# Performance work log

Hardware: AMD Instinct MI355X
Metric: run time of the kernel (lower is better)

## Reference

```python
import jax, jax.numpy as jnp
import numpy as np

N = 50000
E = 800000
IN_C = 128
HID = 64
HEADS = 4
EPS = 1e-5
NEG_SLOPE = 0.2


def _glorot(key, shape, fan_in):
    return jax.random.normal(key, shape, dtype=jnp.float32) / np.sqrt(fan_in)


def setup_inputs() -> dict:
    key = jax.random.key(0)
    ks = jax.random.split(key, 32)
    d = {}
    d["x"] = jax.random.normal(ks[0], (N, IN_C), dtype=jnp.float32)
    d["edge_index"] = jax.random.randint(ks[1], (2, E), 0, N, dtype=jnp.int32)
    ph = HID // HEADS  # per-head channels for concat layers (16)
    # Layer 1: in -> [heads, ph], concat
    d["W1"] = _glorot(ks[2], (IN_C, HEADS * ph), IN_C)
    d["a1s"] = _glorot(ks[3], (HEADS, ph), ph)
    d["a1d"] = _glorot(ks[4], (HEADS, ph), ph)
    d["b1"] = jnp.zeros((HID,), jnp.float32)
    # Layer 2: hid -> [heads, ph], concat
    d["W2"] = _glorot(ks[5], (HID, HEADS * ph), HID)
    d["a2s"] = _glorot(ks[6], (HEADS, ph), ph)
    d["a2d"] = _glorot(ks[7], (HEADS, ph), ph)
    d["b2"] = jnp.zeros((HID,), jnp.float32)
    # Layer 3: hid -> [heads, HID], mean over heads (concat=False)
    d["W3"] = _glorot(ks[8], (HID, HEADS * HID), HID)
    d["a3s"] = _glorot(ks[9], (HEADS, HID), HID)
    d["a3d"] = _glorot(ks[10], (HEADS, HID), HID)
    d["b3"] = jnp.zeros((HID,), jnp.float32)
    # BatchNorms (eval mode: running stats)
    for i, k0 in zip((1, 2, 3), (11, 14, 17)):
        d[f"bn{i}_g"] = jnp.ones((HID,), jnp.float32)
        d[f"bn{i}_b"] = jnp.zeros((HID,), jnp.float32)
        d[f"bn{i}_m"] = 0.1 * jax.random.normal(ks[k0], (HID,), dtype=jnp.float32)
        d[f"bn{i}_v"] = jax.random.uniform(ks[k0 + 1], (HID,), minval=0.5, maxval=1.5, dtype=jnp.float32)
    # Classifier MLP: HID -> HID//2 -> 1
    d["cW1"] = _glorot(ks[20], (HID, HID // 2), HID)
    d["cb1"] = jnp.zeros((HID // 2,), jnp.float32)
    d["cW2"] = _glorot(ks[21], (HID // 2, 1), HID // 2)
    d["cb2"] = jnp.zeros((1,), jnp.float32)
    return d


def _gat_layer(x, src, dst, W, a_s, a_d, b, concat):
    n = x.shape[0]
    heads, outc = a_s.shape
    h = (x @ W).reshape(n, heads, outc)           # [N,H,C]
    al_s = jnp.einsum("nhc,hc->nh", h, a_s)       # [N,H]
    al_d = jnp.einsum("nhc,hc->nh", h, a_d)
    e = jax.nn.leaky_relu(al_s[src] + al_d[dst], NEG_SLOPE)  # [E,H]
    m = jax.ops.segment_max(e, dst, num_segments=n)
    ex = jnp.exp(e - m[dst])
    den = jax.ops.segment_sum(ex, dst, num_segments=n)
    alpha = ex / den[dst]                          # segment softmax over dst
    out = jax.ops.segment_sum(h[src] * alpha[..., None], dst, num_segments=n)  # [N,H,C]
    if concat:
        out = out.reshape(n, heads * outc)
    else:
        out = out.mean(axis=1)
    return out + b


def _bn(x, g, b, m, v):
    return g * (x - m) * jax.lax.rsqrt(v + EPS) + b


def reference(x, edge_index, W1, a1s, a1d, b1, W2, a2s, a2d, b2, W3, a3s, a3d, b3,
              bn1_g, bn1_b, bn1_m, bn1_v, bn2_g, bn2_b, bn2_m, bn2_v,
              bn3_g, bn3_b, bn3_m, bn3_v, cW1, cb1, cW2, cb2):
    n = x.shape[0]
    # PyG GATConv adds self-loops by default
    loop = jnp.arange(n, dtype=edge_index.dtype)
    src = jnp.concatenate([edge_index[0], loop])
    dst = jnp.concatenate([edge_index[1], loop])

    h = _gat_layer(x, src, dst, W1, a1s, a1d, b1, concat=True)
    h = jax.nn.elu(_bn(h, bn1_g, bn1_b, bn1_m, bn1_v))
    h = _gat_layer(h, src, dst, W2, a2s, a2d, b2, concat=True)
    h = jax.nn.elu(_bn(h, bn2_g, bn2_b, bn2_m, bn2_v))
    h = _gat_layer(h, src, dst, W3, a3s, a3d, b3, concat=False)
    h = _bn(h, bn3_g, bn3_b, bn3_m, bn3_v)

    h = jax.nn.elu(h @ cW1 + cb1)
    out = (h @ cW2 + cb2).squeeze(-1)  # [N]
    return out
```

## Files before the change

kernel.cpp:

```cpp
#include <hip/hip_runtime.h>

#define HH 4

__device__ __forceinline__ float lrelu(float v){ return v > 0.f ? v : 0.2f*v; }

template<int IC>
__global__ void gemm_gat(const float* __restrict__ X, const float* __restrict__ W,
                         const float* __restrict__ a_s, const float* __restrict__ a_d,
                         float* __restrict__ h, float* __restrict__ als, float* __restrict__ ald,
                         int N) {
    int t = threadIdx.x, lane = t & 63, wid = t >> 6;
    int n = blockIdx.x*4 + wid;
    bool valid = n < N;
    int nc = valid ? n : N-1;
    __shared__ float xs[4][IC];
    #pragma unroll
    for (int k = lane; k < IC; k += 64) xs[wid][k] = X[(size_t)nc*IC + k];
    float acc = 0.f;
    #pragma unroll 8
    for (int k = 0; k < IC; ++k) acc += xs[wid][k] * W[k*64 + lane];
    if (valid) h[(size_t)nc*64 + lane] = acc;
    int hh = lane >> 4, c = lane & 15;
    float ps = acc * a_s[hh*16 + c];
    float pd = acc * a_d[hh*16 + c];
    #pragma unroll
    for (int m = 1; m < 16; m <<= 1){ ps += __shfl_xor(ps, m); pd += __shfl_xor(pd, m); }
    if (valid && c == 0){ als[nc*HH + hh] = ps; ald[nc*HH + hh] = pd; }
}


__global__ void zero_i32(int* __restrict__ p, int n){
    int i = blockIdx.x*256 + threadIdx.x;
    if (i < n) p[i] = 0;
}

__global__ void count_deg(const int* __restrict__ ei, int* __restrict__ deg, int E){
    int e = blockIdx.x*256 + threadIdx.x;
    if (e < E) atomicAdd(&deg[ei[E + e]], 1);
}

__global__ void deg_bsum(const int* __restrict__ deg, int* __restrict__ bsum, int N){
    int t = threadIdx.x;
    int base = blockIdx.x*1024 + t*4;
    int s = 0;
    if (base + 3 < N){
        int4 v = *(const int4*)(deg + base);
        s = v.x + v.y + v.z + v.w;
    } else {
        for (int q = 0; q < 4; ++q) if (base + q < N) s += deg[base + q];
    }
    #pragma unroll
    for (int m = 1; m < 64; m <<= 1) s += __shfl_xor(s, m);
    __shared__ int ws[4];
    if ((t & 63) == 0) ws[t >> 6] = s;
    __syncthreads();
    if (t == 0) bsum[blockIdx.x] = ws[0] + ws[1] + ws[2] + ws[3];
}

__global__ void scan_write(const int* __restrict__ deg, const int* __restrict__ bsum,
                           int* __restrict__ row_off, int* __restrict__ cursor, int N, int E){
    int t = threadIdx.x, bid = blockIdx.x, lane = t & 63, w = t >> 6;
    int base = bid*1024 + t*4;
    int v0 = 0, v1 = 0, v2 = 0, v3 = 0;
    if (base + 3 < N){
        int4 v = *(const int4*)(deg + base);
        v0 = v.x; v1 = v.y; v2 = v.z; v3 = v.w;
    } else {
        if (base     < N) v0 = deg[base];
        if (base + 1 < N) v1 = deg[base + 1];
        if (base + 2 < N) v2 = deg[base + 2];
        if (base + 3 < N) v3 = deg[base + 3];
    }
    int s = v0 + v1 + v2 + v3;
    int x = s;
    #pragma unroll
    for (int d = 1; d < 64; d <<= 1){
        int y = __shfl_up(x, d);
        if (lane >= d) x += y;
    }
    __shared__ int wsum[4];
    __shared__ int boff_s;
    if (lane == 63) wsum[w] = x;
    if (t < 64){
        int o = 0;
        for (int i = t; i < bid; i += 64) o += bsum[i];
        #pragma unroll
        for (int m = 1; m < 64; m <<= 1) o += __shfl_xor(o, m);
        if (t == 0) boff_s = o;
    }
    __syncthreads();
    int woff = 0;
    for (int i = 0; i < w; ++i) woff += wsum[i];
    int o = boff_s + woff + (x - s);
    if (base     < N){ row_off[base]     = o; cursor[base]     = o; o += v0; }
    if (base + 1 < N){ row_off[base + 1] = o; cursor[base + 1] = o; o += v1; }
    if (base + 2 < N){ row_off[base + 2] = o; cursor[base + 2] = o; o += v2; }
    if (base + 3 < N){ row_off[base + 3] = o; cursor[base + 3] = o; o += v3; }
    if (t == 0 && bid == 0) row_off[N] = E;
}

__global__ void fill_csr(const int* __restrict__ ei, int* __restrict__ cursor,
                         int* __restrict__ ssrc, int E){
    int e = blockIdx.x*256 + threadIdx.x;
    if (e < E){
        int d = ei[E + e];
        int p = atomicAdd(&cursor[d], 1);
        ssrc[p] = ei[e];
    }
}

__global__ void prep_l3(const float* __restrict__ W3, const float* __restrict__ a3s,
                        const float* __restrict__ a3d, float* __restrict__ ws3,
                        float* __restrict__ wd3, float* __restrict__ W3p){
    int t = threadIdx.x;
    int hh = t >> 6, k = t & 63;
    float ss = 0.f, sd = 0.f;
    for (int c = 0; c < 64; ++c){
        float w = W3[k*256 + hh*64 + c];
        ss += w * a3s[hh*64 + c];
        sd += w * a3d[hh*64 + c];
        W3p[t*64 + c] = 0.25f * w;
    }
    ws3[t] = ss; wd3[t] = sd;
}

__global__ void gat_agg16_l1(const int* __restrict__ row_off, const int* __restrict__ ssrc,
                             const float* __restrict__ als, const float* __restrict__ ald,
                             const float* __restrict__ h, const float* __restrict__ b,
                             const float* __restrict__ g, const float* __restrict__ bb,
                             const float* __restrict__ bm, const float* __restrict__ bv,
                             const float* __restrict__ W2, const float* __restrict__ a2s,
                             const float* __restrict__ a2d, float* __restrict__ h2,
                             float* __restrict__ als2, float* __restrict__ ald2, int N){
    int t = threadIdx.x, lane = t & 63, wid = t >> 6;
    __shared__ float wl[4][16][4];
    __shared__ int   sl[4][16];
    __shared__ __align__(16) float vb[4][64];
    int n = blockIdx.x*4 + wid;
    if (n >= N) return;
    int j  = lane & 15;
    int hh = lane >> 4;
    int cb = lane & 15;
    int gq = lane >> 4;
    int hd = cb >> 2;
    float ad_w = ald[n*HH + hh];
    float v_hd = __expf(lrelu(als[n*HH + hd] + ald[n*HH + hd]));
    int beg = row_off[n], end = row_off[n+1];
    float4 acc = make_float4(0.f, 0.f, 0.f, 0.f);
    if (lane < 16){
        float4 hs = *(const float4*)(h + (size_t)n*64 + cb*4);
        acc.x = v_hd*hs.x; acc.y = v_hd*hs.y; acc.z = v_hd*hs.z; acc.w = v_hd*hs.w;
    }
    float denp = 0.f;
    for (int c16 = beg; c16 < end; c16 += 16){
        int e = c16 + j;
        int s = n; float ev = 0.f;
        if (e < end){ s = ssrc[e]; ev = __expf(lrelu(als[s*HH + hh] + ad_w)); }
        denp += ev;
        wl[wid][j][hh] = ev;
        if (hh == 0) sl[wid][j] = s;
        int   s0 = sl[wid][gq],     s1 = sl[wid][4+gq];
        int   s2 = sl[wid][8+gq],   s3 = sl[wid][12+gq];
        float w0 = wl[wid][gq][hd], w1 = wl[wid][4+gq][hd];
        float w2 = wl[wid][8+gq][hd], w3 = wl[wid][12+gq][hd];
        float4 h0 = *(const float4*)(h + (size_t)s0*64 + cb*4);
        float4 h1 = *(const float4*)(h + (size_t)s1*64 + cb*4);
        float4 h2v = *(const float4*)(h + (size_t)s2*64 + cb*4);
        float4 h3 = *(const float4*)(h + (size_t)s3*64 + cb*4);
        acc.x += w0*h0.x + w1*h1.x + w2*h2v.x + w3*h3.x;
        acc.y += w0*h0.y + w1*h1.y + w2*h2v.y + w3*h3.y;
        acc.z += w0*h0.z + w1*h1.z + w2*h2v.z + w3*h3.z;
        acc.w += w0*h0.w + w1*h1.w + w2*h2v.w + w3*h3.w;
    }
    #pragma unroll
    for (int m = 1; m < 16; m <<= 1) denp += __shfl_xor(denp, m);
    float den = __shfl(denp, hd << 4) + v_hd;
    #pragma unroll
    for (int m = 16; m < 64; m <<= 1){
        acc.x += __shfl_xor(acc.x, m); acc.y += __shfl_xor(acc.y, m);
        acc.z += __shfl_xor(acc.z, m); acc.w += __shfl_xor(acc.w, m);
    }
    float4 bb4 = *(const float4*)(b  + cb*4);
    float4 gg4 = *(const float4*)(g  + cb*4);
    float4 be4 = *(const float4*)(bb + cb*4);
    float4 bm4 = *(const float4*)(bm + cb*4);
    float4 bv4 = *(const float4*)(bv + cb*4);
    float4 val;
    val.x = gg4.x*(acc.x/den + bb4.x - bm4.x)*rsqrtf(bv4.x + 1e-5f) + be4.x;
    val.y = gg4.y*(acc.y/den + bb4.y - bm4.y)*rsqrtf(bv4.y + 1e-5f) + be4.y;
    val.z = gg4.z*(acc.z/den + bb4.z - bm4.z)*rsqrtf(bv4.z + 1e-5f) + be4.z;
    val.w = gg4.w*(acc.w/den + bb4.w - bm4.w)*rsqrtf(bv4.w + 1e-5f) + be4.w;
    val.x = val.x > 0.f ? val.x : expm1f(val.x);
    val.y = val.y > 0.f ? val.y : expm1f(val.y);
    val.z = val.z > 0.f ? val.z : expm1f(val.z);
    val.w = val.w > 0.f ? val.w : expm1f(val.w);
    if (lane < 16) *(float4*)&vb[wid][cb*4] = val;
    float acc2 = 0.f;
    #pragma unroll 8
    for (int k = 0; k < 64; ++k) acc2 += vb[wid][k] * W2[k*64 + lane];
    h2[(size_t)n*64 + lane] = acc2;
    float ps = acc2 * a2s[hh*16 + j];
    float pd = acc2 * a2d[hh*16 + j];
    #pragma unroll
    for (int m = 1; m < 16; m <<= 1){ ps += __shfl_xor(ps, m); pd += __shfl_xor(pd, m); }
    if (j == 0){ als2[n*HH + hh] = ps; ald2[n*HH + hh] = pd; }
}

__global__ void gat_agg16_l2(const int* __restrict__ row_off, const int* __restrict__ ssrc,
                             const float* __restrict__ als, const float* __restrict__ ald,
                             const float* __restrict__ h, const float* __restrict__ b,
                             const float* __restrict__ g, const float* __restrict__ bb,
                             const float* __restrict__ bm, const float* __restrict__ bv,
                             float* __restrict__ out,
                             const float* __restrict__ ws3, const float* __restrict__ wd3,
                             float* __restrict__ als3, float* __restrict__ ald3, int N){
    int t = threadIdx.x, lane = t & 63, wid = t >> 6;
    int n = blockIdx.x*4 + wid;
    if (n >= N) return;
    __shared__ float wl[4][16][4];
    __shared__ int   sl[4][16];
    int j  = lane & 15;
    int hh = lane >> 4;
    int cb = lane & 15;
    int gq = lane >> 4;
    int hd = cb >> 2;
    float ad_w = ald[n*HH + hh];
    float v_hd = __expf(lrelu(als[n*HH + hd] + ald[n*HH + hd]));
    int beg = row_off[n], end = row_off[n+1];
    float4 acc = make_float4(0.f, 0.f, 0.f, 0.f);
    if (lane < 16){
        float4 hs = *(const float4*)(h + (size_t)n*64 + cb*4);
        acc.x = v_hd*hs.x; acc.y = v_hd*hs.y; acc.z = v_hd*hs.z; acc.w = v_hd*hs.w;
    }
    float denp = 0.f;
    for (int c16 = beg; c16 < end; c16 += 16){
        int e = c16 + j;
        int s = n; float ev = 0.f;
        if (e < end){ s = ssrc[e]; ev = __expf(lrelu(als[s*HH + hh] + ad_w)); }
        denp += ev;
        wl[wid][j][hh] = ev;
        if (hh == 0) sl[wid][j] = s;
        int   s0 = sl[wid][gq],     s1 = sl[wid][4+gq];
        int   s2 = sl[wid][8+gq],   s3 = sl[wid][12+gq];
        float w0 = wl[wid][gq][hd], w1 = wl[wid][4+gq][hd];
        float w2 = wl[wid][8+gq][hd], w3 = wl[wid][12+gq][hd];
        float4 h0 = *(const float4*)(h + (size_t)s0*64 + cb*4);
        float4 h1 = *(const float4*)(h + (size_t)s1*64 + cb*4);
        float4 h2v = *(const float4*)(h + (size_t)s2*64 + cb*4);
        float4 h3 = *(const float4*)(h + (size_t)s3*64 + cb*4);
        acc.x += w0*h0.x + w1*h1.x + w2*h2v.x + w3*h3.x;
        acc.y += w0*h0.y + w1*h1.y + w2*h2v.y + w3*h3.y;
        acc.z += w0*h0.z + w1*h1.z + w2*h2v.z + w3*h3.z;
        acc.w += w0*h0.w + w1*h1.w + w2*h2v.w + w3*h3.w;
    }
    #pragma unroll
    for (int m = 1; m < 16; m <<= 1) denp += __shfl_xor(denp, m);
    float den = __shfl(denp, hd << 4) + v_hd;
    #pragma unroll
    for (int m = 16; m < 64; m <<= 1){
        acc.x += __shfl_xor(acc.x, m); acc.y += __shfl_xor(acc.y, m);
        acc.z += __shfl_xor(acc.z, m); acc.w += __shfl_xor(acc.w, m);
    }
    float4 bb4 = *(const float4*)(b  + cb*4);
    float4 gg4 = *(const float4*)(g  + cb*4);
    float4 be4 = *(const float4*)(bb + cb*4);
    float4 bm4 = *(const float4*)(bm + cb*4);
    float4 bv4 = *(const float4*)(bv + cb*4);
    float4 val;
    val.x = gg4.x*(acc.x/den + bb4.x - bm4.x)*rsqrtf(bv4.x + 1e-5f) + be4.x;
    val.y = gg4.y*(acc.y/den + bb4.y - bm4.y)*rsqrtf(bv4.y + 1e-5f) + be4.y;
    val.z = gg4.z*(acc.z/den + bb4.z - bm4.z)*rsqrtf(bv4.z + 1e-5f) + be4.z;
    val.w = gg4.w*(acc.w/den + bb4.w - bm4.w)*rsqrtf(bv4.w + 1e-5f) + be4.w;
    val.x = val.x > 0.f ? val.x : expm1f(val.x);
    val.y = val.y > 0.f ? val.y : expm1f(val.y);
    val.z = val.z > 0.f ? val.z : expm1f(val.z);
    val.w = val.w > 0.f ? val.w : expm1f(val.w);
    if (lane < 16) *(float4*)(out + (size_t)n*64 + cb*4) = val;
    float4 w_s = *(const float4*)(ws3 + gq*64 + cb*4);
    float4 w_d = *(const float4*)(wd3 + gq*64 + cb*4);
    float ps = val.x*w_s.x + val.y*w_s.y + val.z*w_s.z + val.w*w_s.w;
    float pd = val.x*w_d.x + val.y*w_d.y + val.z*w_d.z + val.w*w_d.w;
    #pragma unroll
    for (int m = 1; m < 16; m <<= 1){ ps += __shfl_xor(ps, m); pd += __shfl_xor(pd, m); }
    if (cb == 0){ als3[n*HH + gq] = ps; ald3[n*HH + gq] = pd; }
}

__global__ void gat_agg3_fused(const int* __restrict__ row_off, const int* __restrict__ ssrc,
                               const float* __restrict__ als, const float* __restrict__ ald,
                               const float* __restrict__ hin, const float* __restrict__ W3p,
                               const float* __restrict__ b, const float* __restrict__ g,
                               const float* __restrict__ bb, const float* __restrict__ bm,
                               const float* __restrict__ bv, float* __restrict__ out, int N){
    int t = threadIdx.x, lane = t & 63, wid = t >> 6;
    int n0 = blockIdx.x*4;
    int n = min(n0 + wid, N-1);
    __shared__ __align__(16) float buf[4][256];
    __shared__ __align__(16) float ysh[4*256];
    float (*wlp)[4] = (float(*)[4])&buf[wid][0];
    int*  slp       = (int*)&buf[wid][64];
    int j = lane & 15, hh = lane >> 4;
    int cb = lane & 15, gq = lane >> 4;
    float4 adv = *(const float4*)(ald + n*4);
    float4 av  = *(const float4*)(als + n*4);
    float v0 = __expf(lrelu(av.x + adv.x)), v1 = __expf(lrelu(av.y + adv.y));
    float v2 = __expf(lrelu(av.z + adv.z)), v3 = __expf(lrelu(av.w + adv.w));
    float ad_h = hh == 0 ? adv.x : hh == 1 ? adv.y : hh == 2 ? adv.z : adv.w;
    int beg = row_off[n], end = row_off[n+1];
    float4 acc0 = make_float4(0,0,0,0), acc1 = acc0, acc2 = acc0, acc3 = acc0;
    if (lane < 16){
        float4 hs = *(const float4*)(hin + (size_t)n*64 + cb*4);
        acc0.x = v0*hs.x; acc0.y = v0*hs.y; acc0.z = v0*hs.z; acc0.w = v0*hs.w;
        acc1.x = v1*hs.x; acc1.y = v1*hs.y; acc1.z = v1*hs.z; acc1.w = v1*hs.w;
        acc2.x = v2*hs.x; acc2.y = v2*hs.y; acc2.z = v2*hs.z; acc2.w = v2*hs.w;
        acc3.x = v3*hs.x; acc3.y = v3*hs.y; acc3.z = v3*hs.z; acc3.w = v3*hs.w;
    }
    float denp = 0.f;
    for (int c16 = beg; c16 < end; c16 += 16){
        int e = c16 + j;
        int s = n; float ev = 0.f;
        if (e < end){ s = ssrc[e]; ev = __expf(lrelu(als[s*4 + hh] + ad_h)); }
        denp += ev;
        wlp[j][hh] = ev;
        if (hh == 0) slp[j] = s;
        int   sA = slp[gq],      sB = slp[4+gq];
        int   sC = slp[8+gq],    sD = slp[12+gq];
        float4 wA = *(const float4*)wlp[gq];
        float4 wB = *(const float4*)wlp[4+gq];
        float4 wC = *(const float4*)wlp[8+gq];
        float4 wD = *(const float4*)wlp[12+gq];
        float4 hA = *(const float4*)(hin + (size_t)sA*64 + cb*4);
        float4 hB = *(const float4*)(hin + (size_t)sB*64 + cb*4);
        float4 hC = *(const float4*)(hin + (size_t)sC*64 + cb*4);
        float4 hD = *(const float4*)(hin + (size_t)sD*64 + cb*4);
        acc0.x += wA.x*hA.x + wB.x*hB.x + wC.x*hC.x + wD.x*hD.x;
        acc0.y += wA.x*hA.y + wB.x*hB.y + wC.x*hC.y + wD.x*hD.y;
        acc0.z += wA.x*hA.z + wB.x*hB.z + wC.x*hC.z + wD.x*hD.z;
        acc0.w += wA.x*hA.w + wB.x*hB.w + wC.x*hC.w + wD.x*hD.w;
        acc1.x += wA.y*hA.x + wB.y*hB.x + wC.y*hC.x + wD.y*hD.x;
        acc1.y += wA.y*hA.y + wB.y*hB.y + wC.y*hC.y + wD.y*hD.y;
        acc1.z += wA.y*hA.z + wB.y*hB.z + wC.y*hC.z + wD.y*hD.z;
        acc1.w += wA.y*hA.w + wB.y*hB.w + wC.y*hC.w + wD.y*hD.w;
        acc2.x += wA.z*hA.x + wB.z*hB.x + wC.z*hC.x + wD.z*hD.x;
        acc2.y += wA.z*hA.y + wB.z*hB.y + wC.z*hC.y + wD.z*hD.y;
        acc2.z += wA.z*hA.z + wB.z*hB.z + wC.z*hC.z + wD.z*hD.z;
        acc2.w += wA.z*hA.w + wB.z*hB.w + wC.z*hC.w + wD.z*hD.w;
        acc3.x += wA.w*hA.x + wB.w*hB.x + wC.w*hC.x + wD.w*hD.x;
        acc3.y += wA.w*hA.y + wB.w*hB.y + wC.w*hC.y + wD.w*hD.y;
        acc3.z += wA.w*hA.z + wB.w*hB.z + wC.w*hC.z + wD.w*hD.z;
        acc3.w += wA.w*hA.w + wB.w*hB.w + wC.w*hC.w + wD.w*hD.w;
    }
    #pragma unroll
    for (int m = 1; m < 16; m <<= 1) denp += __shfl_xor(denp, m);
    float d0 = v0 + __shfl(denp, 0);
    float d1 = v1 + __shfl(denp, 16);
    float d2 = v2 + __shfl(denp, 32);
    float d3 = v3 + __shfl(denp, 48);
    #pragma unroll
    for (int m = 16; m < 64; m <<= 1){
        acc0.x += __shfl_xor(acc0.x, m); acc0.y += __shfl_xor(acc0.y, m);
        acc0.z += __shfl_xor(acc0.z, m); acc0.w += __shfl_xor(acc0.w, m);
        acc1.x += __shfl_xor(acc1.x, m); acc1.y += __shfl_xor(acc1.y, m);
        acc1.z += __shfl_xor(acc1.z, m); acc1.w += __shfl_xor(acc1.w, m);
        acc2.x += __shfl_xor(acc2.x, m); acc2.y += __shfl_xor(acc2.y, m);
        acc2.z += __shfl_xor(acc2.z, m); acc2.w += __shfl_xor(acc2.w, m);
        acc3.x += __shfl_xor(acc3.x, m); acc3.y += __shfl_xor(acc3.y, m);
        acc3.z += __shfl_xor(acc3.z, m); acc3.w += __shfl_xor(acc3.w, m);
    }
    if (lane < 16){
        float r0 = 1.f/d0, r1 = 1.f/d1, r2 = 1.f/d2, r3 = 1.f/d3;
        *(float4*)&ysh[wid*256 +   0 + cb*4] = make_float4(acc0.x*r0, acc0.y*r0, acc0.z*r0, acc0.w*r0);
        *(float4*)&ysh[wid*256 +  64 + cb*4] = make_float4(acc1.x*r1, acc1.y*r1, acc1.z*r1, acc1.w*r1);
        *(float4*)&ysh[wid*256 + 128 + cb*4] = make_float4(acc2.x*r2, acc2.y*r2, acc2.z*r2, acc2.w*r2);
        *(float4*)&ysh[wid*256 + 192 + cb*4] = make_float4(acc3.x*r3, acc3.y*r3, acc3.z*r3, acc3.w*r3);
    }
    __syncthreads();
    float a0 = 0.f, a1 = 0.f, a2 = 0.f, a3 = 0.f;
    int jbase = wid*64;
    #pragma unroll 4
    for (int jj = 0; jj < 64; jj += 4){
        int jb = jbase + jj;
        float4 y0 = *(const float4*)&ysh[0*256 + jb];
        float4 y1 = *(const float4*)&ysh[1*256 + jb];
        float4 y2 = *(const float4*)&ysh[2*256 + jb];
        float4 y3 = *(const float4*)&ysh[3*256 + jb];
        float w0 = W3p[(jb    )*64 + lane];
        float w1 = W3p[(jb + 1)*64 + lane];
        float w2 = W3p[(jb + 2)*64 + lane];
        float w3 = W3p[(jb + 3)*64 + lane];
        a0 += y0.x*w0 + y0.y*w1 + y0.z*w2 + y0.w*w3;
        a1 += y1.x*w0 + y1.y*w1 + y1.z*w2 + y1.w*w3;
        a2 += y2.x*w0 + y2.y*w1 + y2.z*w2 + y2.w*w3;
        a3 += y3.x*w0 + y3.y*w1 + y3.z*w2 + y3.w*w3;
    }
    buf[wid][0*64 + lane] = a0;
    buf[wid][1*64 + lane] = a1;
    buf[wid][2*64 + lane] = a2;
    buf[wid][3*64 + lane] = a3;
    __syncthreads();
    int nw = n0 + wid;
    if (nw < N){
        float val = buf[0][wid*64 + lane] + buf[1][wid*64 + lane] +
                    buf[2][wid*64 + lane] + buf[3][wid*64 + lane] + b[lane];
        out[(size_t)nw*64 + lane] = g[lane]*(val - bm[lane])*rsqrtf(bv[lane] + 1e-5f) + bb[lane];
    }
}

__global__ void classifier(const float* __restrict__ hin, const float* __restrict__ cW1,
                           const float* __restrict__ cb1, const float* __restrict__ cW2,
                           const float* __restrict__ cb2, float* __restrict__ out, int N){
    __shared__ float w1[64*32];
    __shared__ float b1s[32], w2[32];
    int t = threadIdx.x;
    for (int k = t; k < 64*32; k += 256) w1[k] = cW1[k];
    if (t < 32) { b1s[t] = cb1[t]; w2[t] = cW2[t]; }
    __syncthreads();
    int n = blockIdx.x*256 + t;
    if (n >= N) return;
    float hrow[64];
    #pragma unroll
    for (int k = 0; k < 64; ++k) hrow[k] = hin[(size_t)n*64 + k];
    float acc2 = cb2[0];
    #pragma unroll 4
    for (int j = 0; j < 32; ++j) {
        float a = b1s[j];
        #pragma unroll
        for (int k = 0; k < 64; ++k) a += hrow[k]*w1[k*32 + j];
        float e = a > 0.f ? a : expm1f(a);
        acc2 += e * w2[j];
    }
    out[n] = acc2;
}

extern "C" void kernel_launch(void* const* d_in, const int* in_sizes, int n_in,
                              void* d_out, int out_size, void* d_ws, size_t ws_size,
                              hipStream_t stream) {
    const float* x    = (const float*)d_in[0];
    const int*   ei   = (const int*)  d_in[1];
    const float* W1   = (const float*)d_in[2];
    const float* a1s  = (const float*)d_in[3];
    const float* a1d  = (const float*)d_in[4];
    const float* b1   = (const float*)d_in[5];
    const float* W2   = (const float*)d_in[6];
    const float* a2s  = (const float*)d_in[7];
    const float* a2d  = (const float*)d_in[8];
    const float* b2   = (const float*)d_in[9];
    const float* W3   = (const float*)d_in[10];
    const float* a3s  = (const float*)d_in[11];
    const float* a3d  = (const float*)d_in[12];
    const float* b3   = (const float*)d_in[13];
    const float* bn1g = (const float*)d_in[14];
    const float* bn1b = (const float*)d_in[15];
    const float* bn1m = (const float*)d_in[16];
    const float* bn1v = (const float*)d_in[17];
    const float* bn2g = (const float*)d_in[18];
    const float* bn2b = (const float*)d_in[19];
    const float* bn2m = (const float*)d_in[20];
    const float* bn2v = (const float*)d_in[21];
    const float* bn3g = (const float*)d_in[22];
    const float* bn3b = (const float*)d_in[23];
    const float* bn3m = (const float*)d_in[24];
    const float* bn3v = (const float*)d_in[25];
    const float* cW1  = (const float*)d_in[26];
    const float* cb1  = (const float*)d_in[27];
    const float* cW2  = (const float*)d_in[28];
    const float* cb2  = (const float*)d_in[29];

    const int N = in_sizes[0] / 128;
    const int E = in_sizes[1] / 2;

    float* h    = (float*)d_ws;
    float* h2   = h    + (size_t)N*64;
    float* hin  = h2   + (size_t)N*64;
    float* als  = hin  + (size_t)N*64;
    float* ald  = als  + (size_t)N*4;
    float* als2 = ald  + (size_t)N*4;
    float* ald2 = als2 + (size_t)N*4;
    float* als3 = ald2 + (size_t)N*4;
    float* ald3 = als3 + (size_t)N*4;
    float* ws3  = ald3 + (size_t)N*4;
    float* wd3  = ws3  + 256;
    float* W3p  = wd3  + 256;
    int* deg     = (int*)(W3p + 16384);
    int* row_off = deg + N;
    int* cursor  = row_off + (N + 1);
    int* ssrc    = cursor + N;
    int* bsum    = ssrc + E;

    const int B = 256;
    int gN  = (N + B-1)/B;
    int gE  = (E + B-1)/B;
    int NB  = (N + 1023)/1024;
    int gN4 = (N + 3)/4;

    zero_i32<<<gN, B, 0, stream>>>(deg, N);
    count_deg<<<gE, B, 0, stream>>>(ei, deg, E);
    deg_bsum<<<NB, B, 0, stream>>>(deg, bsum, N);
    scan_write<<<NB, B, 0, stream>>>(deg, bsum, row_off, cursor, N, E);
    fill_csr<<<gE, B, 0, stream>>>(ei, cursor, ssrc, E);
    prep_l3<<<1, 256, 0, stream>>>(W3, a3s, a3d, ws3, wd3, W3p);

    gemm_gat<128><<<gN4, B, 0, stream>>>(x, W1, a1s, a1d, h, als, ald, N);

    gat_agg16_l1<<<gN4, B, 0, stream>>>(row_off, ssrc, als, ald, h, b1,
                                        bn1g, bn1b, bn1m, bn1v,
                                        W2, a2s, a2d, h2, als2, ald2, N);

    gat_agg16_l2<<<gN4, B, 0, stream>>>(row_off, ssrc, als2, ald2, h2, b2,
                                        bn2g, bn2b, bn2m, bn2v, hin,
                                        ws3, wd3, als3, ald3, N);

    gat_agg3_fused<<<gN4, B, 0, stream>>>(row_off, ssrc, als3, ald3, hin, W3p,
                                          b3, bn3g, bn3b, bn3m, bn3v, h, N);

    classifier<<<gN, B, 0, stream>>>(h, cW1, cb1, cW2, cb2, (float*)d_out, N);
}
```

Before: 388.7 us.

## Sort nodes by degree bucket to balance aggregation wavefronts

Builds a degree histogram (capped at 63), scans it, and fills a permutation that groups nodes of similar in-degree. The three aggregation kernels then process nodes in this permuted order, so the wavefronts in a block and nearby blocks see similar edge counts and diverge less in loop trip count. This adds three small kernels and an indirection per node, and it scatters the output and neighbour-feature accesses into non-contiguous node order, which may hurt locality.

```diff
diff --git a/kernel.cpp b/kernel.cpp
--- a/kernel.cpp
+++ b/kernel.cpp
@@ -109,6 +109,32 @@
     }
 }
 
+__global__ void bucket_hist(const int* __restrict__ deg, int* __restrict__ hist, int N){
+    int n = blockIdx.x*256 + threadIdx.x;
+    if (n < N) atomicAdd(&hist[min(deg[n], 63)], 1);
+}
+
+__global__ void bucket_scan(const int* __restrict__ hist, int* __restrict__ bcur){
+    int t = threadIdx.x;
+    int c = hist[t];
+    int x = c;
+    #pragma unroll
+    for (int d = 1; d < 64; d <<= 1){
+        int y = __shfl_up(x, d);
+        if (t >= d) x += y;
+    }
+    bcur[t] = x - c;
+}
+
+__global__ void perm_fill(const int* __restrict__ deg, int* __restrict__ bcur,
+                          int* __restrict__ perm, int N){
+    int n = blockIdx.x*256 + threadIdx.x;
+    if (n < N){
+        int p = atomicAdd(&bcur[min(deg[n], 63)], 1);
+        perm[p] = n;
+    }
+}
+
 __global__ void prep_l3(const float* __restrict__ W3, const float* __restrict__ a3s,
                         const float* __restrict__ a3d, float* __restrict__ ws3,
                         float* __restrict__ wd3, float* __restrict__ W3p){
@@ -124,7 +150,8 @@
     ws3[t] = ss; wd3[t] = sd;
 }
 
-__global__ void gat_agg16_l1(const int* __restrict__ row_off, const int* __restrict__ ssrc,
+__global__ void gat_agg16_l1(const int* __restrict__ perm,
+                             const int* __restrict__ row_off, const int* __restrict__ ssrc,
                              const float* __restrict__ als, const float* __restrict__ ald,
                              const float* __restrict__ h, const float* __restrict__ b,
                              const float* __restrict__ g, const float* __restrict__ bb,
@@ -136,8 +163,9 @@
     __shared__ float wl[4][16][4];
     __shared__ int   sl[4][16];
     __shared__ __align__(16) float vb[4][64];
-    int n = blockIdx.x*4 + wid;
-    if (n >= N) return;
+    int idx = blockIdx.x*4 + wid;
+    if (idx >= N) return;
+    int n = perm[idx];
     int j  = lane & 15;
     int hh = lane >> 4;
     int cb = lane & 15;
@@ -206,7 +234,8 @@
     if (j == 0){ als2[n*HH + hh] = ps; ald2[n*HH + hh] = pd; }
 }
 
-__global__ void gat_agg16_l2(const int* __restrict__ row_off, const int* __restrict__ ssrc,
+__global__ void gat_agg16_l2(const int* __restrict__ perm,
+                             const int* __restrict__ row_off, const int* __restrict__ ssrc,
                              const float* __restrict__ als, const float* __restrict__ ald,
                              const float* __restrict__ h, const float* __restrict__ b,
                              const float* __restrict__ g, const float* __restrict__ bb,
@@ -215,8 +244,9 @@
                              const float* __restrict__ ws3, const float* __restrict__ wd3,
                              float* __restrict__ als3, float* __restrict__ ald3, int N){
     int t = threadIdx.x, lane = t & 63, wid = t >> 6;
-    int n = blockIdx.x*4 + wid;
-    if (n >= N) return;
+    int idx = blockIdx.x*4 + wid;
+    if (idx >= N) return;
+    int n = perm[idx];
     __shared__ float wl[4][16][4];
     __shared__ int   sl[4][16];
     int j  = lane & 15;
@@ -285,15 +315,16 @@
     if (cb == 0){ als3[n*HH + gq] = ps; ald3[n*HH + gq] = pd; }
 }
 
-__global__ void gat_agg3_fused(const int* __restrict__ row_off, const int* __restrict__ ssrc,
+__global__ void gat_agg3_fused(const int* __restrict__ perm,
+                               const int* __restrict__ row_off, const int* __restrict__ ssrc,
                                const float* __restrict__ als, const float* __restrict__ ald,
                                const float* __restrict__ hin, const float* __restrict__ W3p,
                                const float* __restrict__ b, const float* __restrict__ g,
                                const float* __restrict__ bb, const float* __restrict__ bm,
                                const float* __restrict__ bv, float* __restrict__ out, int N){
     int t = threadIdx.x, lane = t & 63, wid = t >> 6;
-    int n0 = blockIdx.x*4;
-    int n = min(n0 + wid, N-1);
+    int idx = blockIdx.x*4 + wid;
+    int n = perm[min(idx, N-1)];
     __shared__ __align__(16) float buf[4][256];
     __shared__ __align__(16) float ysh[4*256];
     float (*wlp)[4] = (float(*)[4])&buf[wid][0];
@@ -397,11 +428,10 @@
     buf[wid][2*64 + lane] = a2;
     buf[wid][3*64 + lane] = a3;
     __syncthreads();
-    int nw = n0 + wid;
-    if (nw < N){
+    if (idx < N){
         float val = buf[0][wid*64 + lane] + buf[1][wid*64 + lane] +
                     buf[2][wid*64 + lane] + buf[3][wid*64 + lane] + b[lane];
-        out[(size_t)nw*64 + lane] = g[lane]*(val - bm[lane])*rsqrtf(bv[lane] + 1e-5f) + bb[lane];
+        out[(size_t)n*64 + lane] = g[lane]*(val - bm[lane])*rsqrtf(bv[lane] + 1e-5f) + bb[lane];
     }
 }
 
@@ -484,32 +514,39 @@
     int* row_off = deg + N;
     int* cursor  = row_off + (N + 1);
     int* ssrc    = cursor + N;
+    int NB_      = (N + 1023)/1024;
     int* bsum    = ssrc + E;
+    int* hist    = bsum + NB_;
+    int* bcur    = hist + 64;
+    int* perm    = bcur + 64;
 
     const int B = 256;
     int gN  = (N + B-1)/B;
     int gE  = (E + B-1)/B;
-    int NB  = (N + 1023)/1024;
     int gN4 = (N + 3)/4;
 
     zero_i32<<<gN, B, 0, stream>>>(deg, N);
+    zero_i32<<<1, B, 0, stream>>>(hist, 128);
     count_deg<<<gE, B, 0, stream>>>(ei, deg, E);
-    deg_bsum<<<NB, B, 0, stream>>>(deg, bsum, N);
-    scan_write<<<NB, B, 0, stream>>>(deg, bsum, row_off, cursor, N, E);
+    deg_bsum<<<NB_, B, 0, stream>>>(deg, bsum, N);
+    scan_write<<<NB_, B, 0, stream>>>(deg, bsum, row_off, cursor, N, E);
     fill_csr<<<gE, B, 0, stream>>>(ei, cursor, ssrc, E);
+    bucket_hist<<<gN, B, 0, stream>>>(deg, hist, N);
+    bucket_scan<<<1, 64, 0, stream>>>(hist, bcur);
+    perm_fill<<<gN, B, 0, stream>>>(deg, bcur, perm, N);
     prep_l3<<<1, 256, 0, stream>>>(W3, a3s, a3d, ws3, wd3, W3p);
 
     gemm_gat<128><<<gN4, B, 0, stream>>>(x, W1, a1s, a1d, h, als, ald, N);
 
-    gat_agg16_l1<<<gN4, B, 0, stream>>>(row_off, ssrc, als, ald, h, b1,
+    gat_agg16_l1<<<gN4, B, 0, stream>>>(perm, row_off, ssrc, als, ald, h, b1,
                                         bn1g, bn1b, bn1m, bn1v,
                                         W2, a2s, a2d, h2, als2, ald2, N);
 
-    gat_agg16_l2<<<gN4, B, 0, stream>>>(row_off, ssrc, als2, ald2, h2, b2,
+    gat_agg16_l2<<<gN4, B, 0, stream>>>(perm, row_off, ssrc, als2, ald2, h2, b2,
                                         bn2g, bn2b, bn2m, bn2v, hin,
                                         ws3, wd3, als3, ald3, N);
 
-    gat_agg3_fused<<<gN4, B, 0, stream>>>(row_off, ssrc, als3, ald3, hin, W3p,
+    gat_agg3_fused<<<gN4, B, 0, stream>>>(perm, row_off, ssrc, als3, ald3, hin, W3p,
                                           b3, bn3g, bn3b, bn3m, bn3v, h, N);
 
     classifier<<<gN, B, 0, stream>>>(h, cW1, cb1, cW2, cb2, (float*)d_out, N);
```

Result: slower. 677.3 us (+74.3%).
